# Kernel optimization log

Measured on AMD Instinct MI355X. Metric: run time of the kernel, lower is better.

## Reference

```python
import jax, jax.numpy as jnp
import numpy as np
from jax import lax

TEMPERATURE = 0.0005


def conv1d(x, w, b, pad):
    # x: [B, Cin, T], w: [Cout, Cin, K], b: [Cout]
    y = lax.conv_general_dilated(x, w, window_strides=(1,), padding=[(pad, pad)],
                                 dimension_numbers=('NCH', 'OIH', 'NCH'))
    return y + b[None, :, None]


def setup_inputs() -> dict:
    key = jax.random.key(0)
    ks = jax.random.split(key, 16)
    B, Cq, Ck, Ca, Tde, Ten = 32, 80, 512, 80, 2000, 400

    def xavier(k, shape):
        fan_in = shape[1] * (shape[2] if len(shape) > 2 else 1)
        fan_out = shape[0] * (shape[2] if len(shape) > 2 else 1)
        lim = float(np.sqrt(6.0 / (fan_in + fan_out)))
        return jax.random.uniform(k, shape, jnp.float32, -lim, lim)

    inp = {
        'queries': jax.random.normal(ks[0], (B, Cq, Tde), jnp.float32),
        'keys': jax.random.normal(ks[1], (B, Ck, Ten), jnp.float32),
        'mask': jnp.ones((B, 1, Ten), jnp.int32),
        # key_layer: Conv(512->1024,k3,p1) -> ReLU -> Conv(1024->80,k1)
        'kw1': xavier(ks[2], (Ck * 2, Ck, 3)), 'kb1': jnp.zeros((Ck * 2,), jnp.float32),
        'kw2': xavier(ks[3], (Ca, Ck * 2, 1)), 'kb2': jnp.zeros((Ca,), jnp.float32),
        # query_layer: Conv(80->160,k3,p1)->ReLU->Conv(160->80,k1)->ReLU->Conv(80->80,k1)
        'qw1': xavier(ks[4], (Cq * 2, Cq, 3)), 'qb1': jnp.zeros((Cq * 2,), jnp.float32),
        'qw2': xavier(ks[5], (Cq, Cq * 2, 1)), 'qb2': jnp.zeros((Cq,), jnp.float32),
        'qw3': xavier(ks[6], (Ca, Cq, 1)), 'qb3': jnp.zeros((Ca,), jnp.float32),
    }
    return inp


def reference(queries, keys, mask, kw1, kb1, kw2, kb2, qw1, qb1, qw2, qb2, qw3, qb3):
    # key path: conv3 -> relu -> conv1
    k = conv1d(jax.nn.relu(conv1d(keys, kw1, kb1, 1)), kw2, kb2, 0)          # [B,Ca,Ten]
    # query path: conv3 -> relu -> conv1 -> relu -> conv1
    q = conv1d(queries, qw1, qb1, 1)
    q = jax.nn.relu(conv1d(jax.nn.relu(q), qw2, qb2, 0))
    q = conv1d(q, qw3, qb3, 0)                                               # [B,Ca,Tde]

    # sum_c (q - k)^2 = |q|^2 + |k|^2 - 2 q.k  (avoids [B,C,Tde,Ten] intermediate)
    q2 = jnp.sum(q * q, axis=1)                      # [B,Tde]
    k2 = jnp.sum(k * k, axis=1)                      # [B,Ten]
    qk = jnp.einsum('bcd,bce->bde', q, k)            # [B,Tde,Ten]
    dist = q2[:, :, None] + k2[:, None, :] - 2.0 * qk
    attn_logp = (-TEMPERATURE * dist)[:, None]       # [B,1,Tde,Ten]

    # masked fill over encoder positions (softmax dim)
    m = mask.astype(bool)[:, :, None, :]             # [B,1,1,Ten]
    attn_logp = jnp.where(m, attn_logp, -jnp.inf)
    attn = jax.nn.softmax(attn_logp, axis=3)
    return attn, attn_logp
```

## Files before the change

### kernel.cpp

```cpp
#include <hip/hip_runtime.h>
#include <hip/hip_bf16.h>
#include <math.h>

#define NB 32
#define CK 512
#define C1 1024
#define CA 80
#define CQ 80
#define CQ2 160
#define TEN 400
#define TDE 2000
#define KDIM 1536
#define TPAD 448
#define TQP 2048

static constexpr float TEMP = 0.0005f;

typedef __attribute__((ext_vector_type(8))) short short8;
typedef __attribute__((ext_vector_type(4))) float f32x4;

__device__ inline short f2bf(float v) {
  __hip_bfloat16 h = __float2bfloat16(v);
  return *(short*)&h;
}

__device__ inline void gload_lds16(const void* g, void* l) {
  __builtin_amdgcn_global_load_lds(
      (const __attribute__((address_space(1))) unsigned int*)g,
      (__attribute__((address_space(3))) unsigned int*)l, 16, 0, 0);
}

__global__ __launch_bounds__(256) void cvt_w1_kernel(
    const float* __restrict__ w1, short* __restrict__ w1bf) {
  int i = blockIdx.x * 256 + threadIdx.x;
  if (i < C1 * KDIM) w1bf[i] = f2bf(w1[i]);
}

__global__ __launch_bounds__(256) void cvt_pad_kernel(
    const float* __restrict__ src, short* __restrict__ dst,
    int M, int K, int Mp, int Kp) {
  int i = blockIdx.x * 256 + threadIdx.x;
  if (i >= Mp * Kp) return;
  int r = i / Kp, c = i - r * Kp;
  float v = (r < M && c < K) ? src[(size_t)r * K + c] : 0.f;
  dst[i] = f2bf(v);
}

__global__ __launch_bounds__(256) void im2col_kernel(
    const float* __restrict__ keys, short* __restrict__ BmatT) {
  const int t = blockIdx.x;
  const int b = blockIdx.y;
  const int tid = threadIdx.x;
  short* dst = BmatT + ((size_t)b * TPAD + t) * KDIM;
  #pragma unroll
  for (int i = 0; i < 6; ++i) {
    int k = tid + i * 256;
    int ci = k / 3;
    int dk = k - ci * 3;
    int ts = t + dk - 1;
    float v = (ts >= 0 && ts < TEN) ? keys[((size_t)b * CK + ci) * TEN + ts] : 0.f;
    dst[k] = f2bf(v);
  }
}

__global__ __launch_bounds__(256) void im2col_q_kernel(
    const float* __restrict__ queries, short* __restrict__ Bq) {
  const int t = blockIdx.x;
  const int b = blockIdx.y;
  const int k = threadIdx.x;
  float v = 0.f;
  if (t < TDE && k < 240) {
    int ci = k / 3, dk = k - ci * 3, ts = t + dk - 1;
    v = (ts >= 0 && ts < TDE) ? queries[((size_t)b * CQ + ci) * TDE + ts] : 0.f;
  }
  Bq[((size_t)b * TQP + t) * 256 + k] = f2bf(v);
}

__global__ __launch_bounds__(256) void kconv1_mfma_kernel(
    const short* __restrict__ w1bf, const short* __restrict__ BmatT,
    const float* __restrict__ b1, short* __restrict__ k1t) {
  __shared__ short A_lds[4096];
  __shared__ short B_lds[4096];
  const int flat = blockIdx.x;
  const int cox = flat >> 7;
  const int rem = flat & 127;
  const int b   = rem >> 2;
  const int ty  = rem & 3;
  const int co0 = cox * 128;
  const int t0  = ty * 128;
  const int tid = threadIdx.x;
  const int l = tid & 63, w = tid >> 6;

  auto invswz = [](int Y) {
    int X = Y;
    X ^= ((Y >> 8) & 1) << 6;
    X ^= ((Y >> 7) & 1) << 5;
    X ^= (((Y >> 6) ^ (Y >> 8)) & 1) << 4;
    return X;
  };

  const short* gsrc[4];
  short* ldst[4];
  #pragma unroll
  for (int j = 0; j < 4; ++j) {
    int c = w * 4 + j;
    int Y = (c & 7) * 1024 + l * 16;
    int X = invswz(Y);
    int row = X >> 6, slot = (X >> 4) & 3;
    if (c < 8) {
      gsrc[j] = w1bf + (size_t)(co0 + row) * KDIM + slot * 8;
      ldst[j] = &A_lds[(c & 7) * 512];
    } else {
      int gr = t0 + row;
      if (gr > TPAD - 1) gr = TPAD - 1;
      gsrc[j] = BmatT + ((size_t)b * TPAD + gr) * KDIM + slot * 8;
      ldst[j] = &B_lds[(c & 7) * 512];
    }
  }

  const int kslot = l >> 4;
  int abyte[2];
  #pragma unroll
  for (int i = 0; i < 2; ++i) {
    int arow = w * 32 + i * 16 + (l & 15);
    abyte[i] = (arow * 64 + kslot * 16) ^ ((arow & 7) << 4);
  }
  int bbyte[8];
  #pragma unroll
  for (int g = 0; g < 8; ++g) {
    int brow = g * 16 + (l & 15);
    bbyte[g] = (brow * 64 + kslot * 16) ^ ((brow & 7) << 4);
  }

  f32x4 acc[2][8];
  #pragma unroll
  for (int i = 0; i < 2; ++i)
    #pragma unroll
    for (int g = 0; g < 8; ++g) acc[i][g] = (f32x4){0.f, 0.f, 0.f, 0.f};

  for (int kt = 0; kt < KDIM / 32; ++kt) {
    __syncthreads();
    #pragma unroll
    for (int j = 0; j < 4; ++j) gload_lds16(gsrc[j] + kt * 32, ldst[j]);
    __syncthreads();
    short8 a0 = *(const short8*)((const char*)A_lds + abyte[0]);
    short8 a1 = *(const short8*)((const char*)A_lds + abyte[1]);
    #pragma unroll
    for (int g = 0; g < 8; ++g) {
      short8 bb = *(const short8*)((const char*)B_lds + bbyte[g]);
      acc[0][g] = __builtin_amdgcn_mfma_f32_16x16x32_bf16(a0, bb, acc[0][g], 0, 0, 0);
      acc[1][g] = __builtin_amdgcn_mfma_f32_16x16x32_bf16(a1, bb, acc[1][g], 0, 0, 0);
    }
  }

  #pragma unroll
  for (int g = 0; g < 8; ++g) {
    int t = t0 + g * 16 + (l & 15);
    if (t < TEN) {
      #pragma unroll
      for (int i = 0; i < 2; ++i) {
        #pragma unroll
        for (int r = 0; r < 4; ++r) {
          int co = co0 + w * 32 + i * 16 + kslot * 4 + r;
          float v = acc[i][g][r] + b1[co];
          k1t[((size_t)b * TPAD + t) * C1 + co] = f2bf(v > 0.f ? v : 0.f);
        }
      }
    }
  }
}

template <int MODE, bool RELU>
__global__ __launch_bounds__(256) void qgemm_kernel(
    const short* __restrict__ A, const short* __restrict__ B,
    const float* __restrict__ bias, void* __restrict__ outv,
    int M, int Kpad, int kiters, int Nvalid, int outCols,
    size_t bBatchStride, size_t outBatchStride, int outLD) {
  __shared__ short A_lds[2048];
  __shared__ short B_lds[2048];
  const int co0 = blockIdx.x * 64;
  const int t0  = blockIdx.y * 64;
  const int b   = blockIdx.z;
  const int tid = threadIdx.x;
  const int l = tid & 63, w = tid >> 6;
  const int srow = tid >> 2, sslot = tid & 3;

  const short* gA = A + (size_t)(co0 + srow) * Kpad + sslot * 8;
  const short* gB = B + (size_t)b * bBatchStride + (size_t)(t0 + srow) * Kpad + sslot * 8;
  const int wbyte = (srow * 64 + sslot * 16) ^ ((srow & 7) << 4);

  const int kslot = l >> 4;
  const int arow = w * 16 + (l & 15);
  const int abyte = (arow * 64 + kslot * 16) ^ ((arow & 7) << 4);
  int bbyte[4];
  #pragma unroll
  for (int g = 0; g < 4; ++g) {
    int brow = g * 16 + (l & 15);
    bbyte[g] = (brow * 64 + kslot * 16) ^ ((brow & 7) << 4);
  }

  f32x4 acc[4];
  #pragma unroll
  for (int g = 0; g < 4; ++g) acc[g] = (f32x4){0.f, 0.f, 0.f, 0.f};

  uint4 av = *(const uint4*)gA;
  uint4 bv = *(const uint4*)gB;
  for (int kt = 0; kt < kiters; ++kt) {
    __syncthreads();
    *(uint4*)((char*)A_lds + wbyte) = av;
    *(uint4*)((char*)B_lds + wbyte) = bv;
    __syncthreads();
    uint4 an = av, bn = bv;
    if (kt + 1 < kiters) {
      an = *(const uint4*)(gA + (kt + 1) * 32);
      bn = *(const uint4*)(gB + (kt + 1) * 32);
    }
    short8 a = *(const short8*)((const char*)A_lds + abyte);
    #pragma unroll
    for (int g = 0; g < 4; ++g) {
      short8 bb = *(const short8*)((const char*)B_lds + bbyte[g]);
      acc[g] = __builtin_amdgcn_mfma_f32_16x16x32_bf16(a, bb, acc[g], 0, 0, 0);
    }
    av = an; bv = bn;
  }

  #pragma unroll
  for (int g = 0; g < 4; ++g) {
    int t = t0 + g * 16 + (l & 15);
    if (t >= Nvalid) continue;
    #pragma unroll
    for (int r = 0; r < 4; ++r) {
      int co = co0 + w * 16 + kslot * 4 + r;
      if (MODE == 1) {
        if (co < outCols) {
          float v = 0.f;
          if (co < M) {
            v = acc[g][r] + bias[co];
            if (RELU) v = v > 0.f ? v : 0.f;
          }
          ((short*)outv)[(size_t)b * outBatchStride + (size_t)t * outLD + co] = f2bf(v);
        }
      } else {
        if (co < M) {
          float v = acc[g][r] + bias[co];
          if (RELU) v = v > 0.f ? v : 0.f;
          ((float*)outv)[(size_t)b * outBatchStride + (size_t)co * outLD + t] = v;
        }
      }
    }
  }
}

__global__ __launch_bounds__(256) void prep_attn_q_kernel(
    const float* __restrict__ q3, short* __restrict__ qA,
    float* __restrict__ q2) {
  __shared__ float sm[80][64];
  const int b = blockIdx.y;
  const int t0 = blockIdx.x * 64;
  const int tid = threadIdx.x;
  for (int idx = tid; idx < 80 * 64; idx += 256) {
    int a = idx >> 6, j = idx & 63;
    int t = t0 + j;
    sm[a][j] = (t < TDE) ? q3[((size_t)b * CA + a) * TDE + t] : 0.f;
  }
  __syncthreads();
  if (tid < 64) {
    float ss = 0.f;
    #pragma unroll 8
    for (int a = 0; a < 80; ++a) { float v = sm[a][tid]; ss += v * v; }
    q2[(size_t)b * TQP + t0 + tid] = ss;
  }
  for (int idx = tid; idx < 64 * 96; idx += 256) {
    int j = idx / 96, k = idx - j * 96;
    float v = (k < 80) ? sm[k][j] : 0.f;
    qA[((size_t)b * TQP + t0 + j) * 96 + k] = f2bf(v);
  }
}

__global__ __launch_bounds__(256) void prep_attn_k_kernel(
    const float* __restrict__ kfeat, short* __restrict__ kB,
    float* __restrict__ k2) {
  __shared__ float sm[80][64];
  const int b = blockIdx.y;
  const int s0 = blockIdx.x * 64;
  const int tid = threadIdx.x;
  for (int idx = tid; idx < 80 * 64; idx += 256) {
    int a = idx >> 6, j = idx & 63;
    int s = s0 + j;
    sm[a][j] = (s < TEN) ? kfeat[((size_t)b * CA + a) * TEN + s] : 0.f;
  }
  __syncthreads();
  if (tid < 64) {
    float ss = 0.f;
    #pragma unroll 8
    for (int a = 0; a < 80; ++a) { float v = sm[a][tid]; ss += v * v; }
    k2[(size_t)b * TPAD + s0 + tid] = ss;
  }
  for (int idx = tid; idx < 64 * 96; idx += 256) {
    int j = idx / 96, k = idx - j * 96;
    float v = (k < 80) ? sm[k][j] : 0.f;
    kB[((size_t)b * TPAD + s0 + j) * 96 + k] = f2bf(v);
  }
}

__global__ __launch_bounds__(256) void attn_fused_kernel(
    const short* __restrict__ qA, const short* __restrict__ kB,
    const float* __restrict__ q2, const float* __restrict__ k2,
    const int* __restrict__ mask, float* __restrict__ out_attn,
    float* __restrict__ out_logp) {
  __shared__ short A_lds[3][2048];
  __shared__ short B_lds[3][2560];
  __shared__ float k2LDS[400];
  __shared__ int mLDS[400];
  const int t0 = blockIdx.x * 64;
  const int b  = blockIdx.y;
  const int tid = threadIdx.x;
  const int l = tid & 63, w = tid >> 6;

  {
    const int arow_s = tid >> 2, aslot = tid & 3;
    const short* gA = qA + ((size_t)b * TQP + t0 + arow_s) * 96 + aslot * 8;
    #pragma unroll
    for (int p = 0; p < 3; ++p) {
      uint4 v = *(const uint4*)(gA + p * 32);
      *(uint4*)((char*)&A_lds[p][0] +
                ((arow_s * 64 + aslot * 16) ^ ((arow_s & 7) << 4))) = v;
    }
  }
  for (int idx = tid; idx < 400; idx += 256) {
    k2LDS[idx] = k2[(size_t)b * TPAD + idx];
    mLDS[idx] = mask[(size_t)b * TEN + idx];
  }

  const int kslot = l >> 4;
  const int arow = w * 16 + (l & 15);
  const int abyte = (arow * 64 + kslot * 16) ^ ((arow & 7) << 4);

  f32x4 acc[25];
  #pragma unroll
  for (int i = 0; i < 25; ++i) acc[i] = (f32x4){0.f, 0.f, 0.f, 0.f};

  __syncthreads();
  #pragma unroll
  for (int st = 0; st < 5; ++st) {
    for (int idx = tid; idx < 960; idx += 256) {
      int row = idx / 12, c = idx - row * 12;
      int panel = c >> 2, ps = c & 3;
      uint4 v = *(const uint4*)(kB + ((size_t)b * TPAD + st * 80 + row) * 96 + c * 8);
      *(uint4*)((char*)&B_lds[panel][0] +
                ((row * 64 + ps * 16) ^ ((row & 7) << 4))) = v;
    }
    __syncthreads();
    #pragma unroll
    for (int kt = 0; kt < 3; ++kt) {
      short8 a = *(const short8*)((const char*)&A_lds[kt][0] + abyte);
      #pragma unroll
      for (int f = 0; f < 5; ++f) {
        int brow = f * 16 + (l & 15);
        short8 bb = *(const short8*)((const char*)&B_lds[kt][0] +
                                     ((brow * 64 + kslot * 16) ^ ((brow & 7) << 4)));
        acc[st * 5 + f] =
            __builtin_amdgcn_mfma_f32_16x16x32_bf16(a, bb, acc[st * 5 + f], 0, 0, 0);
      }
    }
    __syncthreads();
  }

  int trow[4]; float q2v[4];
  #pragma unroll
  for (int r = 0; r < 4; ++r) {
    trow[r] = t0 + w * 16 + kslot * 4 + r;
    q2v[r] = q2[(size_t)b * TQP + trow[r]];
  }
  #pragma unroll
  for (int sf = 0; sf < 25; ++sf) {
    int s = sf * 16 + (l & 15);
    float k2v = k2LDS[s];
    bool mk = mLDS[s] != 0;
    #pragma unroll
    for (int r = 0; r < 4; ++r) {
      float lp = mk ? (-TEMP) * (q2v[r] + k2v - 2.f * acc[sf][r]) : -INFINITY;
      acc[sf][r] = lp;
    }
  }
  #pragma unroll
  for (int r = 0; r < 4; ++r) {
    if (trow[r] < TDE) {
      float* dst = out_logp + ((size_t)(b * TDE + trow[r])) * TEN + (l & 15);
      #pragma unroll
      for (int sf = 0; sf < 25; ++sf) dst[sf * 16] = acc[sf][r];
    }
  }
  float m[4];
  #pragma unroll
  for (int r = 0; r < 4; ++r) m[r] = -INFINITY;
  #pragma unroll
  for (int sf = 0; sf < 25; ++sf)
    #pragma unroll
    for (int r = 0; r < 4; ++r) m[r] = fmaxf(m[r], acc[sf][r]);
  #pragma unroll
  for (int o = 1; o < 16; o <<= 1)
    #pragma unroll
    for (int r = 0; r < 4; ++r) m[r] = fmaxf(m[r], __shfl_xor(m[r], o, 64));
  float sum[4] = {0.f, 0.f, 0.f, 0.f};
  #pragma unroll
  for (int sf = 0; sf < 25; ++sf)
    #pragma unroll
    for (int r = 0; r < 4; ++r) {
      float v = acc[sf][r];
      float e = (v != -INFINITY) ? __expf(v - m[r]) : 0.f;
      acc[sf][r] = e;
      sum[r] += e;
    }
  #pragma unroll
  for (int o = 1; o < 16; o <<= 1)
    #pragma unroll
    for (int r = 0; r < 4; ++r) sum[r] += __shfl_xor(sum[r], o, 64);
  float inv[4];
  #pragma unroll
  for (int r = 0; r < 4; ++r) inv[r] = 1.0f / sum[r];
  #pragma unroll
  for (int r = 0; r < 4; ++r) {
    if (trow[r] < TDE) {
      float* dst = out_attn + ((size_t)(b * TDE + trow[r])) * TEN + (l & 15);
      #pragma unroll
      for (int sf = 0; sf < 25; ++sf) dst[sf * 16] = acc[sf][r] * inv[r];
    }
  }
}

extern "C" void kernel_launch(void* const* d_in, const int* in_sizes, int n_in,
                              void* d_out, int out_size, void* d_ws, size_t ws_size,
                              hipStream_t stream) {
  const float* queries = (const float*)d_in[0];
  const float* keys    = (const float*)d_in[1];
  const int*   mask    = (const int*)d_in[2];
  const float* kw1 = (const float*)d_in[3];
  const float* kb1 = (const float*)d_in[4];
  const float* kw2 = (const float*)d_in[5];
  const float* kb2 = (const float*)d_in[6];
  const float* qw1 = (const float*)d_in[7];
  const float* qb1 = (const float*)d_in[8];
  const float* qw2 = (const float*)d_in[9];
  const float* qb2 = (const float*)d_in[10];
  const float* qw3 = (const float*)d_in[11];
  const float* qb3 = (const float*)d_in[12];
  float* out = (float*)d_out;

  char* ws = (char*)d_ws;
  short* BmatT = (short*)ws;
  short* w1bf  = (short*)(ws + 44040192);
  short* k1t   = (short*)(ws + 47185920);
  short* w2bf  = (short*)(ws + 76546048);
  short* w1q   = (short*)(ws + 76808192);
  short* w2q   = (short*)(ws + 76906496);
  short* w3q   = (short*)(ws + 76947456);
  short* Bq    = (short*)ws;
  short* q1bf  = (short*)(ws + 33554432);
  short* q2bf  = (short*)(ws + 54525952);
  float* q3    = (float*)ws;
  short* qA    = (short*)(ws + 20480000);
  float* q2n   = (float*)(ws + 33062912);
  short* kB    = (short*)(ws + 47185920);
  float* k2n   = (float*)(ws + 49938432);
  float* kfeat = (float*)(ws + 81920000);

  const long long HALF = 25600000LL;
  float* out_attn = out;
  float* out_logp = out + HALF;

  cvt_w1_kernel<<<dim3((C1 * KDIM + 255) / 256), dim3(256), 0, stream>>>(kw1, w1bf);
  im2col_kernel<<<dim3(TEN, NB), dim3(256), 0, stream>>>(keys, BmatT);
  kconv1_mfma_kernel<<<dim3(1024), dim3(256), 0, stream>>>(w1bf, BmatT, kb1, k1t);
  cvt_pad_kernel<<<dim3((128 * 1024 + 255) / 256), dim3(256), 0, stream>>>(
      kw2, w2bf, CA, C1, 128, C1);
  qgemm_kernel<2, false><<<dim3(2, 7, NB), dim3(256), 0, stream>>>(
      w2bf, k1t, kb2, kfeat, CA, C1, 32, TEN, CA,
      (size_t)TPAD * C1, (size_t)CA * TEN, TEN);

  cvt_pad_kernel<<<dim3((192 * 256 + 255) / 256), dim3(256), 0, stream>>>(
      qw1, w1q, CQ2, 240, 192, 256);
  cvt_pad_kernel<<<dim3((128 * 160 + 255) / 256), dim3(256), 0, stream>>>(
      qw2, w2q, CA, CQ2, 128, 160);
  cvt_pad_kernel<<<dim3((128 * 96 + 255) / 256), dim3(256), 0, stream>>>(
      qw3, w3q, CA, CQ, 128, 96);
  im2col_q_kernel<<<dim3(TQP, NB), dim3(256), 0, stream>>>(queries, Bq);
  qgemm_kernel<1, true><<<dim3(3, TQP / 64, NB), dim3(256), 0, stream>>>(
      w1q, Bq, qb1, q1bf, CQ2, 256, 8, TDE, 160,
      (size_t)TQP * 256, (size_t)TQP * 160, 160);
  qgemm_kernel<1, true><<<dim3(2, TQP / 64, NB), dim3(256), 0, stream>>>(
      w2q, q1bf, qb2, q2bf, CA, 160, 5, TDE, 96,
      (size_t)TQP * 160, (size_t)TQP * 96, 96);
  qgemm_kernel<2, false><<<dim3(2, TQP / 64, NB), dim3(256), 0, stream>>>(
      w3q, q2bf, qb3, q3, CA, 96, 3, TDE, 80,
      (size_t)TQP * 96, (size_t)CA * TDE, TDE);

  prep_attn_q_kernel<<<dim3(TQP / 64, NB), dim3(256), 0, stream>>>(q3, qA, q2n);
  prep_attn_k_kernel<<<dim3(TPAD / 64, NB), dim3(256), 0, stream>>>(kfeat, kB, k2n);
  attn_fused_kernel<<<dim3(TQP / 64, NB), dim3(256), 0, stream>>>(
      qA, kB, q2n, k2n, mask, out_attn, out_logp);
}
```

Measured before the change: 370.3 us.

## Write bf16 attention operands directly from final GEMMs and merge weight conversions

```diff
diff --git a/kernel.cpp b/kernel.cpp
--- a/kernel.cpp
+++ b/kernel.cpp
@@ -23,6 +23,10 @@
   __hip_bfloat16 h = __float2bfloat16(v);
   return *(short*)&h;
 }
+__device__ inline float bf2f(short s) {
+  __hip_bfloat16 h = *(__hip_bfloat16*)&s;
+  return __bfloat162float(h);
+}
 
 __device__ inline void gload_lds16(const void* g, void* l) {
   __builtin_amdgcn_global_load_lds(
@@ -30,20 +34,40 @@
       (__attribute__((address_space(3))) unsigned int*)l, 16, 0, 0);
 }
 
-__global__ __launch_bounds__(256) void cvt_w1_kernel(
-    const float* __restrict__ w1, short* __restrict__ w1bf) {
+__global__ __launch_bounds__(256) void cvt_weights_kernel(
+    const float* __restrict__ kw1, const float* __restrict__ kw2,
+    const float* __restrict__ qw1, const float* __restrict__ qw2,
+    const float* __restrict__ qw3, short* __restrict__ w1bf,
+    short* __restrict__ w2bf, short* __restrict__ w1q,
+    short* __restrict__ w2q, short* __restrict__ w3q) {
   int i = blockIdx.x * 256 + threadIdx.x;
-  if (i < C1 * KDIM) w1bf[i] = f2bf(w1[i]);
-}
-
-__global__ __launch_bounds__(256) void cvt_pad_kernel(
-    const float* __restrict__ src, short* __restrict__ dst,
-    int M, int K, int Mp, int Kp) {
-  int i = blockIdx.x * 256 + threadIdx.x;
-  if (i >= Mp * Kp) return;
-  int r = i / Kp, c = i - r * Kp;
-  float v = (r < M && c < K) ? src[(size_t)r * K + c] : 0.f;
-  dst[i] = f2bf(v);
+  if (i < 1572864) {
+    w1bf[i] = f2bf(kw1[i]);
+    return;
+  }
+  i -= 1572864;
+  if (i < 131072) {
+    int r = i >> 10, c = i & 1023;
+    w2bf[i] = f2bf(r < CA ? kw2[r * 1024 + c] : 0.f);
+    return;
+  }
+  i -= 131072;
+  if (i < 49152) {
+    int r = i >> 8, c = i & 255;
+    w1q[i] = f2bf((r < CQ2 && c < 240) ? qw1[r * 240 + c] : 0.f);
+    return;
+  }
+  i -= 49152;
+  if (i < 20480) {
+    int r = i / 160, c = i - r * 160;
+    w2q[i] = f2bf(r < CA ? qw2[r * 160 + c] : 0.f);
+    return;
+  }
+  i -= 20480;
+  if (i < 12288) {
+    int r = i / 96, c = i - r * 96;
+    w3q[i] = f2bf((r < CA && c < CQ) ? qw3[r * 80 + c] : 0.f);
+  }
 }
 
 __global__ __launch_bounds__(256) void im2col_kernel(
@@ -251,56 +275,36 @@
   }
 }
 
-__global__ __launch_bounds__(256) void prep_attn_q_kernel(
-    const float* __restrict__ q3, short* __restrict__ qA,
-    float* __restrict__ q2) {
-  __shared__ float sm[80][64];
-  const int b = blockIdx.y;
-  const int t0 = blockIdx.x * 64;
+__global__ __launch_bounds__(256) void norms_kernel(
+    const short* __restrict__ qA, const short* __restrict__ kB,
+    float* __restrict__ q2n, float* __restrict__ k2n) {
   const int tid = threadIdx.x;
-  for (int idx = tid; idx < 80 * 64; idx += 256) {
-    int a = idx >> 6, j = idx & 63;
-    int t = t0 + j;
-    sm[a][j] = (t < TDE) ? q3[((size_t)b * CA + a) * TDE + t] : 0.f;
-  }
-  __syncthreads();
-  if (tid < 64) {
-    float ss = 0.f;
-    #pragma unroll 8
-    for (int a = 0; a < 80; ++a) { float v = sm[a][tid]; ss += v * v; }
-    q2[(size_t)b * TQP + t0 + tid] = ss;
-  }
-  for (int idx = tid; idx < 64 * 96; idx += 256) {
-    int j = idx / 96, k = idx - j * 96;
-    float v = (k < 80) ? sm[k][j] : 0.f;
-    qA[((size_t)b * TQP + t0 + j) * 96 + k] = f2bf(v);
-  }
-}
-
-__global__ __launch_bounds__(256) void prep_attn_k_kernel(
-    const float* __restrict__ kfeat, short* __restrict__ kB,
-    float* __restrict__ k2) {
-  __shared__ float sm[80][64];
-  const int b = blockIdx.y;
-  const int s0 = blockIdx.x * 64;
-  const int tid = threadIdx.x;
-  for (int idx = tid; idx < 80 * 64; idx += 256) {
-    int a = idx >> 6, j = idx & 63;
-    int s = s0 + j;
-    sm[a][j] = (s < TEN) ? kfeat[((size_t)b * CA + a) * TEN + s] : 0.f;
-  }
-  __syncthreads();
-  if (tid < 64) {
-    float ss = 0.f;
-    #pragma unroll 8
-    for (int a = 0; a < 80; ++a) { float v = sm[a][tid]; ss += v * v; }
-    k2[(size_t)b * TPAD + s0 + tid] = ss;
-  }
-  for (int idx = tid; idx < 64 * 96; idx += 256) {
-    int j = idx / 96, k = idx - j * 96;
-    float v = (k < 80) ? sm[k][j] : 0.f;
-    kB[((size_t)b * TPAD + s0 + j) * 96 + k] = f2bf(v);
-  }
+  const int R = blockIdx.x * 64 + (tid >> 2);
+  const int g = tid & 3;
+  const short* src;
+  float* dst;
+  if (R < NB * TQP) {
+    src = qA + (size_t)R * 96 + g * 24;
+    dst = q2n + R;
+  } else {
+    int R2 = R - NB * TQP;
+    if (R2 >= NB * TPAD) return;
+    src = kB + (size_t)R2 * 96 + g * 24;
+    dst = k2n + R2;
+  }
+  float s = 0.f;
+  #pragma unroll
+  for (int c = 0; c < 3; ++c) {
+    short8 v = *(const short8*)(src + c * 8);
+    #pragma unroll
+    for (int j = 0; j < 8; ++j) {
+      float f = bf2f(v[j]);
+      s += f * f;
+    }
+  }
+  s += __shfl_xor(s, 1, 64);
+  s += __shfl_xor(s, 2, 64);
+  if (g == 0) *dst = s;
 }
 
 __global__ __launch_bounds__(256) void attn_fused_kernel(
@@ -458,45 +462,37 @@
   short* Bq    = (short*)ws;
   short* q1bf  = (short*)(ws + 33554432);
   short* q2bf  = (short*)(ws + 54525952);
-  float* q3    = (float*)ws;
   short* qA    = (short*)(ws + 20480000);
   float* q2n   = (float*)(ws + 33062912);
-  short* kB    = (short*)(ws + 47185920);
   float* k2n   = (float*)(ws + 49938432);
-  float* kfeat = (float*)(ws + 81920000);
+  short* kB    = (short*)(ws + 81920000);
 
   const long long HALF = 25600000LL;
   float* out_attn = out;
   float* out_logp = out + HALF;
 
-  cvt_w1_kernel<<<dim3((C1 * KDIM + 255) / 256), dim3(256), 0, stream>>>(kw1, w1bf);
+  cvt_weights_kernel<<<dim3(6976), dim3(256), 0, stream>>>(
+      kw1, kw2, qw1, qw2, qw3, w1bf, w2bf, w1q, w2q, w3q);
+
   im2col_kernel<<<dim3(TEN, NB), dim3(256), 0, stream>>>(keys, BmatT);
   kconv1_mfma_kernel<<<dim3(1024), dim3(256), 0, stream>>>(w1bf, BmatT, kb1, k1t);
-  cvt_pad_kernel<<<dim3((128 * 1024 + 255) / 256), dim3(256), 0, stream>>>(
-      kw2, w2bf, CA, C1, 128, C1);
-  qgemm_kernel<2, false><<<dim3(2, 7, NB), dim3(256), 0, stream>>>(
-      w2bf, k1t, kb2, kfeat, CA, C1, 32, TEN, CA,
-      (size_t)TPAD * C1, (size_t)CA * TEN, TEN);
-
-  cvt_pad_kernel<<<dim3((192 * 256 + 255) / 256), dim3(256), 0, stream>>>(
-      qw1, w1q, CQ2, 240, 192, 256);
-  cvt_pad_kernel<<<dim3((128 * 160 + 255) / 256), dim3(256), 0, stream>>>(
-      qw2, w2q, CA, CQ2, 128, 160);
-  cvt_pad_kernel<<<dim3((128 * 96 + 255) / 256), dim3(256), 0, stream>>>(
-      qw3, w3q, CA, CQ, 128, 96);
+  qgemm_kernel<1, false><<<dim3(2, 7, NB), dim3(256), 0, stream>>>(
+      w2bf, k1t, kb2, kB, CA, C1, 32, TEN, 96,
+      (size_t)TPAD * C1, (size_t)TPAD * 96, 96);
+
   im2col_q_kernel<<<dim3(TQP, NB), dim3(256), 0, stream>>>(queries, Bq);
   qgemm_kernel<1, true><<<dim3(3, TQP / 64, NB), dim3(256), 0, stream>>>(
-      w1q, Bq, qb1, q1bf, CQ2, 256, 8, TDE, 160,
+      w1q, Bq, qb1, q1bf, CQ2, 256, 8, TQP, 160,
       (size_t)TQP * 256, (size_t)TQP * 160, 160);
   qgemm_kernel<1, true><<<dim3(2, TQP / 64, NB), dim3(256), 0, stream>>>(
-      w2q, q1bf, qb2, q2bf, CA, 160, 5, TDE, 96,
+      w2q, q1bf, qb2, q2bf, CA, 160, 5, TQP, 96,
       (size_t)TQP * 160, (size_t)TQP * 96, 96);
-  qgemm_kernel<2, false><<<dim3(2, TQP / 64, NB), dim3(256), 0, stream>>>(
-      w3q, q2bf, qb3, q3, CA, 96, 3, TDE, 80,
-      (size_t)TQP * 96, (size_t)CA * TDE, TDE);
-
-  prep_attn_q_kernel<<<dim3(TQP / 64, NB), dim3(256), 0, stream>>>(q3, qA, q2n);
-  prep_attn_k_kernel<<<dim3(TPAD / 64, NB), dim3(256), 0, stream>>>(kfeat, kB, k2n);
+  qgemm_kernel<1, false><<<dim3(2, TQP / 64, NB), dim3(256), 0, stream>>>(
+      w3q, q2bf, qb3, qA, CA, 96, 3, TQP, 96,
+      (size_t)TQP * 96, (size_t)TQP * 96, 96);
+
+  norms_kernel<<<dim3((NB * TQP + NB * TPAD) / 64), dim3(256), 0, stream>>>(
+      qA, kB, q2n, k2n);
   attn_fused_kernel<<<dim3(TQP / 64, NB), dim3(256), 0, stream>>>(
       qA, kB, q2n, k2n, mask, out_attn, out_logp);
 }
```

Result: faster. 344.8 us, median of 2 (-6.9%).
